# Performance work log

Measured on AMD Instinct MI355X. Metric: run time of the kernel, lower is better.

## Reference

```python
import jax, jax.numpy as jnp
import numpy as np

EPS = 1e-5
NUM_MEM_TOKENS = 16
SEGMENT_SIZE = 512


def dpfp(x):
    # DPFP feature map (Schlag et al.), nu=1: doubles the last dim, all-nonnegative.
    x2 = jnp.concatenate([jax.nn.relu(x), jax.nn.relu(-x)], axis=-1)
    return x2 * jnp.roll(x2, 1, axis=-1)


def setup_inputs() -> dict:
    key = jax.random.key(0)
    ks = jax.random.split(key, 7)
    B, S, D, DM = 4, 4224, 1024, 64  # S = n_seg * (segment_size + num_mem_tokens) = 8*528
    scale = 0.02
    return {
        "hidden_states": jax.random.normal(ks[0], (B, S, D), jnp.float32),
        "model_output": jax.random.normal(ks[1], (B, S, D), jnp.float32),
        "W_mq": jax.random.normal(ks[2], (D, DM), jnp.float32) * scale,
        "W_mk": jax.random.normal(ks[3], (D, DM), jnp.float32) * scale,
        "W_mv": jax.random.normal(ks[4], (D, D), jnp.float32) * scale,
        "W_mb": jax.random.normal(ks[5], (D, D), jnp.float32) * scale,
        "b_mb": jnp.zeros((D,), jnp.float32),
    }


def reference(hidden_states, model_output, W_mq, W_mk, W_mv, W_mb, b_mb):
    B, S, D = hidden_states.shape
    L = SEGMENT_SIZE + NUM_MEM_TOKENS
    n_seg = S // L
    d_key = 2 * W_mq.shape[1]  # dpfp doubles feature dim

    # [n_seg, B, L, D]
    h = hidden_states.reshape(B, n_seg, L, D).transpose(1, 0, 2, 3)
    m = model_output.reshape(B, n_seg, L, D).transpose(1, 0, 2, 3)

    def step(carry, seg):
        W_mem, z = carry  # [B, d_key, D], [B, d_key]
        hid, mo = seg     # [B, L, D] each
        # --- associate: linear-attention read of compressive memory ---
        q = dpfp(hid @ W_mq)                                   # [B, L, d_key]
        num = jnp.einsum('blk,bkd->bld', q, W_mem)             # [B, L, D]
        den = jnp.einsum('blk,bk->bl', q, z)[..., None] + EPS
        assoc = num / den
        # --- delta-rule memory update from memory tokens of segment output ---
        mem = (assoc + mo)[:, -NUM_MEM_TOKENS:]                # [B, M, D]
        k = dpfp(mem @ W_mk)                                   # [B, M, d_key]
        v = mem @ W_mv                                         # [B, M, D]
        gate = jax.nn.sigmoid(mem @ W_mb + b_mb)               # [B, M, D]
        prev = jnp.einsum('bmk,bkd->bmd', k, W_mem) / (
            jnp.einsum('bmk,bk->bm', k, z)[..., None] + EPS)   # correction (old value)
        new_info = gate * (v - prev)
        W_mem = W_mem + jnp.einsum('bmk,bmd->bkd', k, new_info)
        z = z + k.sum(axis=1)
        return (W_mem, z), assoc

    W0 = jnp.zeros((B, d_key, D), hidden_states.dtype)
    z0 = jnp.zeros((B, d_key), hidden_states.dtype)
    _, assocs = jax.lax.scan(step, (W0, z0), (h, m))           # [n_seg, B, L, D]
    association = jnp.tanh(assocs.transpose(1, 0, 2, 3).reshape(B, S, D))
    return model_output + association
```

## Files before the change

### kernel.cpp

```cpp
#include <hip/hip_runtime.h>
#include <hip/hip_bf16.h>

#define EPS 1e-5f

typedef short s8v __attribute__((ext_vector_type(8)));
typedef short s4v __attribute__((ext_vector_type(4)));
typedef float f4v __attribute__((ext_vector_type(4)));

__device__ __forceinline__ unsigned short f2bf(float f) {
  unsigned u = __builtin_bit_cast(unsigned, f);
  u = u + 0x7FFFu + ((u >> 16) & 1u);
  return (unsigned short)(u >> 16);
}
__device__ __forceinline__ float bf2f(unsigned short h) {
  unsigned u = ((unsigned)h) << 16;
  return __builtin_bit_cast(float, u);
}
__device__ __forceinline__ float fast_tanh(float x) {
  float e = __expf(2.0f * x);
  return 1.0f - 2.0f / (e + 1.0f);
}
__device__ __forceinline__ float fast_sigmoid(float x) {
  return 1.0f / (1.0f + __expf(-x));
}
__device__ __forceinline__ float frcp(float x) { return __builtin_amdgcn_rcpf(x); }

__global__ __launch_bounds__(256) void transpose_kernel(
    const float* __restrict__ W_mq, const float* __restrict__ W_mk,
    const float* __restrict__ W_mv, const float* __restrict__ W_mb,
    unsigned short* __restrict__ W_mqT, unsigned short* __restrict__ W_mkT,
    unsigned short* __restrict__ W_mvT, unsigned short* __restrict__ W_mbT) {
  __shared__ float tile[32][33];
  int bid = blockIdx.x;
  const float* src; unsigned short* dst; int N, t0;
  if (bid < 64)        { src = W_mq; dst = W_mqT; N = 64;   t0 = bid; }
  else if (bid < 128)  { src = W_mk; dst = W_mkT; N = 64;   t0 = bid - 64; }
  else if (bid < 1152) { src = W_mv; dst = W_mvT; N = 1024; t0 = bid - 128; }
  else                 { src = W_mb; dst = W_mbT; N = 1024; t0 = bid - 1152; }
  const int K = 1024;
  int tk = t0 & 31, tn = t0 >> 5;
  int k0 = tk * 32, n0 = tn * 32;
  int t = threadIdx.x;
  int cr = t >> 5, cc = t & 31;
#pragma unroll
  for (int u = 0; u < 4; u++) {
    int row = cr + u * 8;
    tile[row][cc] = src[(size_t)(k0 + row) * N + n0 + cc];
  }
  __syncthreads();
#pragma unroll
  for (int u = 0; u < 4; u++) {
    int nl = cr + u * 8;
    dst[(size_t)(n0 + nl) * K + k0 + cc] = f2bf(tile[cc][nl]);
  }
}

__global__ __launch_bounds__(128) void q_kernel(
    const float* __restrict__ HS, const unsigned short* __restrict__ W_mqT,
    unsigned short* __restrict__ Q) {
  __shared__ __align__(16) union { float y[16 * 64]; unsigned short kq[16 * 128]; } lds;
  int t = threadIdx.x, wv = t >> 6, lane = t & 63, m = lane & 15, q = lane >> 4;
  int r0 = blockIdx.x * 16;
  const float* ap = HS + (size_t)(r0 + m) * 1024 + wv * 512 + q * 8;
  const unsigned short* bp = W_mqT + (size_t)m * 1024 + wv * 512 + q * 8;
  f4v acc[4] = {f4v{0,0,0,0}, f4v{0,0,0,0}, f4v{0,0,0,0}, f4v{0,0,0,0}};
#pragma unroll 4
  for (int ks = 0; ks < 16; ks++) {
    int k0 = ks * 32;
    f4v h0 = *(const f4v*)(ap + k0);
    f4v h1 = *(const f4v*)(ap + k0 + 4);
    s8v a;
    a[0] = (short)f2bf(h0[0]); a[1] = (short)f2bf(h0[1]);
    a[2] = (short)f2bf(h0[2]); a[3] = (short)f2bf(h0[3]);
    a[4] = (short)f2bf(h1[0]); a[5] = (short)f2bf(h1[1]);
    a[6] = (short)f2bf(h1[2]); a[7] = (short)f2bf(h1[3]);
#pragma unroll
    for (int nf = 0; nf < 4; nf++) {
      s8v b = *(const s8v*)(bp + nf * 16384 + k0);
      acc[nf] = __builtin_amdgcn_mfma_f32_16x16x32_bf16(a, b, acc[nf], 0, 0, 0);
    }
  }
  if (wv == 1) {
#pragma unroll
    for (int nf = 0; nf < 4; nf++)
#pragma unroll
      for (int i = 0; i < 4; i++)
        lds.y[(nf * 4 + i) * 64 + lane] = acc[nf][i];
  }
  __syncthreads();
  if (wv == 0) {
#pragma unroll
    for (int nf = 0; nf < 4; nf++)
#pragma unroll
      for (int i = 0; i < 4; i++)
        acc[nf][i] += lds.y[(nf * 4 + i) * 64 + lane];
    int srcl = (lane & 48) | ((m + 15) & 15);
#pragma unroll
    for (int i = 0; i < 4; i++) {
      float yp[4];
#pragma unroll
      for (int nf = 0; nf < 4; nf++) yp[nf] = __shfl(acc[nf][i], srcl);
      int r = q * 4 + i;
#pragma unroll
      for (int nf = 0; nf < 4; nf++) {
        float yv = acc[nf][i];
        float py = (m != 0) ? yp[nf] : (nf > 0 ? yp[nf - 1] : yp[3]);
        bool wrap = (m == 0 && nf == 0);
        float x2lo = wrap ? fmaxf(-py, 0.f) : fmaxf(py, 0.f);
        float x2hi = wrap ? fmaxf(py, 0.f) : fmaxf(-py, 0.f);
        lds.kq[r * 128 + nf * 16 + m]      = f2bf(fmaxf(yv, 0.f) * x2lo);
        lds.kq[r * 128 + 64 + nf * 16 + m] = f2bf(fmaxf(-yv, 0.f) * x2hi);
      }
    }
  }
  __syncthreads();
  {
    int row = t >> 3, ch = t & 7;
    unsigned short* qp = Q + (size_t)(r0 + row) * 128 + ch * 16;
    *(s8v*)(qp)     = *(const s8v*)&lds.kq[row * 128 + ch * 16];
    *(s8v*)(qp + 8) = *(const s8v*)&lds.kq[row * 128 + ch * 16 + 8];
  }
}

__global__ __launch_bounds__(256, 1) void scan_kernel(
    const unsigned short* __restrict__ Qb, const unsigned short* __restrict__ W_mkT,
    const unsigned short* __restrict__ W_mvT, const unsigned short* __restrict__ W_mbT,
    const float* __restrict__ b_mb, const float* __restrict__ MO,
    float* __restrict__ OUT, unsigned short* __restrict__ hist,
    float* __restrict__ zh, unsigned short* __restrict__ mem_bf, int* bar) {
  __shared__ float Wf[128 * 64];
  __shared__ __align__(16) unsigned short Wbf[64 * 132];
  __shared__ float y_lds[16 * 64];
  __shared__ __align__(16) float k_f[16 * 128];
  __shared__ __align__(16) unsigned short k_bf[16 * 136];
  __shared__ float kden_l[16];
  __shared__ float ni_lds[16 * 65];
  __shared__ float z_l[128];

  int t = threadIdx.x, wv = t >> 6, lane = t & 63, m = lane & 15, q = lane >> 4;
  int ct = blockIdx.x & 15, b = blockIdx.x >> 4;
  int col = ct * 64 + wv * 16 + m;

  for (int i = t; i < 128 * 64; i += 256) Wf[i] = 0.f;
  for (int i = t; i < 64 * 132; i += 256) Wbf[i] = 0;
  if (t < 128) z_l[t] = 0.f;
  float bmb = b_mb[col];
  __syncthreads();

  s8v aq[4]; float mo_pf[4];
  {
    const unsigned short* qp = Qb + ((size_t)b * 4224 + 512 + m) * 128;
#pragma unroll
    for (int ks = 0; ks < 4; ks++) aq[ks] = *(const s8v*)(qp + ks * 32 + q * 8);
    const float* mop = MO + ((size_t)b * 4224 + 512 + q * 4) * 1024 + col;
#pragma unroll
    for (int i = 0; i < 4; i++) mo_pf[i] = mop[(size_t)i * 1024];
  }

  for (int s = 0; s < 8; s++) {
    {
      float dp = 0.f;
#pragma unroll
      for (int ks = 0; ks < 4; ks++)
#pragma unroll
        for (int j = 0; j < 8; j++)
          dp += bf2f((unsigned short)aq[ks][j]) * z_l[ks * 32 + q * 8 + j];
      dp += __shfl_xor(dp, 16);
      dp += __shfl_xor(dp, 32);
      dp += EPS;
      f4v acc = {0, 0, 0, 0};
#pragma unroll
      for (int ks = 0; ks < 4; ks++) {
        s8v bv = *(const s8v*)&Wbf[(wv * 16 + m) * 132 + ks * 32 + q * 8];
        acc = __builtin_amdgcn_mfma_f32_16x16x32_bf16(aq[ks], bv, acc, 0, 0, 0);
      }
      unsigned short* mb = mem_bf + (s & 1) * 65536 + b * 16384;
      size_t grow = (size_t)b * 4224 + s * 528 + 512;
#pragma unroll
      for (int i = 0; i < 4; i++) {
        float rden = frcp(__shfl(dp, q * 4 + i));
        float assoc = acc[i] * rden;
        float mov = mo_pf[i];
        OUT[(grow + q * 4 + i) * 1024 + col] = mov + fast_tanh(assoc);
        mb[(q * 4 + i) * 1024 + col] = f2bf(assoc + mov);
      }
    }
    __syncthreads();
    if (t == 0) {
      __threadfence();
      atomicAdd(bar + s * 4 + b, 1);
      while (__hip_atomic_load(bar + s * 4 + b, __ATOMIC_RELAXED,
                               __HIP_MEMORY_SCOPE_AGENT) < 16)
        __builtin_amdgcn_s_sleep(1);
      __threadfence();
    }
    __syncthreads();
    f4v accv = {0,0,0,0}, accg = {0,0,0,0};
    {
      const unsigned short* avp = mem_bf + (s & 1) * 65536 + b * 16384 + m * 1024 + q * 8;
      const unsigned short* bkp = W_mkT + (size_t)(wv * 16 + m) * 1024 + q * 8;
      const unsigned short* bvp = W_mvT + (size_t)col * 1024 + q * 8;
      const unsigned short* bgp = W_mbT + (size_t)col * 1024 + q * 8;
      f4v acy = {0, 0, 0, 0};
#pragma unroll 4
      for (int ks = 0; ks < 32; ks++) {
        s8v av = *(const s8v*)(avp + ks * 32);
        s8v bk = *(const s8v*)(bkp + ks * 32);
        s8v bv = *(const s8v*)(bvp + ks * 32);
        s8v bg = *(const s8v*)(bgp + ks * 32);
        acy  = __builtin_amdgcn_mfma_f32_16x16x32_bf16(av, bk, acy, 0, 0, 0);
        accv = __builtin_amdgcn_mfma_f32_16x16x32_bf16(av, bv, accv, 0, 0, 0);
        accg = __builtin_amdgcn_mfma_f32_16x16x32_bf16(av, bg, accg, 0, 0, 0);
      }
#pragma unroll
      for (int i = 0; i < 4; i++) y_lds[(q * 4 + i) * 64 + wv * 16 + m] = acy[i];
    }
    __syncthreads();
    {
      int r = t >> 4, jg = t & 15;
      const float* yr = &y_lds[r * 64];
      float pd = 0.f;
#pragma unroll
      for (int u = 0; u < 8; u++) {
        int jj = jg * 8 + u, jm = (jj + 127) & 127;
        float yj = (jj < 64) ? yr[jj] : -yr[jj - 64];
        float ym = (jm < 64) ? yr[jm] : -yr[jm - 64];
        float kv = fmaxf(yj, 0.f) * fmaxf(ym, 0.f);
        k_f[r * 128 + jj] = kv;
        k_bf[r * 136 + jj] = f2bf(kv);
        pd += kv * z_l[jj];
      }
      pd += __shfl_xor(pd, 1);
      pd += __shfl_xor(pd, 2);
      pd += __shfl_xor(pd, 4);
      pd += __shfl_xor(pd, 8);
      if (jg == 0) kden_l[r] = pd + EPS;
    }
    __syncthreads();
    {
      f4v accp = {0, 0, 0, 0};
#pragma unroll
      for (int ks = 0; ks < 4; ks++) {
        s8v ak = *(const s8v*)&k_bf[m * 136 + ks * 32 + q * 8];
        s8v bm = *(const s8v*)&Wbf[(wv * 16 + m) * 132 + ks * 32 + q * 8];
        accp = __builtin_amdgcn_mfma_f32_16x16x32_bf16(ak, bm, accp, 0, 0, 0);
      }
#pragma unroll
      for (int i = 0; i < 4; i++) {
        int r = q * 4 + i;
        float prev = accp[i] * frcp(kden_l[r]);
        float g = fast_sigmoid(accg[i] + bmb);
        ni_lds[r * 65 + wv * 16 + m] = g * (accv[i] - prev);
      }
      if (t < 128) {
        float ssum = 0.f;
#pragma unroll
        for (int r = 0; r < 16; r++) ssum += k_f[r * 128 + t];
        z_l[t] += ssum;
        if (s < 7) zh[(s + 1) * 512 + b * 128 + t] = z_l[t];
      }
    }
    __syncthreads();
    {
      int cl = t & 63, kg = t >> 6;
      float niv[16];
#pragma unroll
      for (int mm = 0; mm < 16; mm++) niv[mm] = ni_lds[mm * 65 + cl];
      float delta[32];
#pragma unroll
      for (int jj = 0; jj < 32; jj++) delta[jj] = 0.f;
#pragma unroll
      for (int mm = 0; mm < 16; mm++) {
        const float* kb = &k_f[mm * 128 + kg * 32];
        float nv = niv[mm];
#pragma unroll
        for (int ch = 0; ch < 8; ch++) {
          f4v kv4 = *(const f4v*)(kb + ch * 4);
#pragma unroll
          for (int jj = 0; jj < 4; jj++) delta[ch * 4 + jj] += kv4[jj] * nv;
        }
      }
      unsigned short* hdst = hist + (size_t)(s + 1) * 524288 +
                             ((size_t)b * 1024 + ct * 64 + cl) * 128 + kg * 32;
#pragma unroll
      for (int c8 = 0; c8 < 4; c8++) {
        s8v pk;
#pragma unroll
        for (int u = 0; u < 8; u++) {
          int kk = kg * 32 + c8 * 8 + u;
          float nv = Wf[kk * 64 + cl] + delta[c8 * 8 + u];
          Wf[kk * 64 + cl] = nv;
          pk[u] = (short)f2bf(nv);
        }
        *(s8v*)&Wbf[cl * 132 + kg * 32 + c8 * 8] = pk;
        if (s < 7) *(s8v*)(hdst + c8 * 8) = pk;
      }
      if (s < 7) {
        const unsigned short* qp = Qb + ((size_t)b * 4224 + (s + 1) * 528 + 512 + m) * 128;
#pragma unroll
        for (int ks = 0; ks < 4; ks++) aq[ks] = *(const s8v*)(qp + ks * 32 + q * 8);
        const float* mop = MO + ((size_t)b * 4224 + (s + 1) * 528 + 512 + q * 4) * 1024 + col;
#pragma unroll
        for (int i = 0; i < 4; i++) mo_pf[i] = mop[(size_t)i * 1024];
      }
    }
    __syncthreads();
  }
}

__global__ __launch_bounds__(256) void a_bulk_kernel(
    const unsigned short* __restrict__ Qb, const unsigned short* __restrict__ hist,
    const float* __restrict__ zh, const float* __restrict__ MO,
    float* __restrict__ OUT) {
  __shared__ float as_l[64 * 65];
  int t = threadIdx.x, wv = t >> 6, lane = t & 63, m = lane & 15, q = lane >> 4;
  int rt4 = blockIdx.x, ct = blockIdx.y;
  int seg = blockIdx.z >> 2, b = blockIdx.z & 3;
  const unsigned short* Wm = hist + (size_t)seg * 524288 + ((size_t)b * 1024 + ct * 64) * 128;
  const float* zp = zh + seg * 512 + b * 128;
  size_t grow = (size_t)b * 4224 + seg * 528 + rt4 * 64 + wv * 16;
  const unsigned short* qp = Qb + (grow + m) * 128;
  s8v a[4];
  float dp = 0.f;
#pragma unroll
  for (int ks = 0; ks < 4; ks++) {
    a[ks] = *(const s8v*)(qp + ks * 32 + q * 8);
    f4v z0 = *(const f4v*)(zp + ks * 32 + q * 8);
    f4v z1 = *(const f4v*)(zp + ks * 32 + q * 8 + 4);
#pragma unroll
    for (int j = 0; j < 4; j++) dp += bf2f((unsigned short)a[ks][j]) * z0[j];
#pragma unroll
    for (int j = 0; j < 4; j++) dp += bf2f((unsigned short)a[ks][j + 4]) * z1[j];
  }
  dp += __shfl_xor(dp, 16);
  dp += __shfl_xor(dp, 32);
  dp += EPS;
  f4v acc[4] = {f4v{0,0,0,0}, f4v{0,0,0,0}, f4v{0,0,0,0}, f4v{0,0,0,0}};
#pragma unroll
  for (int ks = 0; ks < 4; ks++) {
#pragma unroll
    for (int nf = 0; nf < 4; nf++) {
      s8v bv = *(const s8v*)(Wm + (size_t)(nf * 16 + m) * 128 + ks * 32 + q * 8);
      acc[nf] = __builtin_amdgcn_mfma_f32_16x16x32_bf16(a[ks], bv, acc[nf], 0, 0, 0);
    }
  }
#pragma unroll
  for (int i = 0; i < 4; i++) {
    float rden = frcp(__shfl(dp, q * 4 + i));
#pragma unroll
    for (int nf = 0; nf < 4; nf++)
      as_l[(wv * 16 + q * 4 + i) * 65 + nf * 16 + m] = acc[nf][i] * rden;
  }
  __syncthreads();
  {
    int r = t >> 2, cchunk = (t & 3) * 16;
    size_t rbase = ((size_t)b * 4224 + seg * 528 + rt4 * 64 + r) * 1024 + ct * 64 + cchunk;
    const float* ar = &as_l[r * 65 + cchunk];
#pragma unroll
    for (int u = 0; u < 4; u++) {
      f4v mo = *(const f4v*)(MO + rbase + u * 4);
      f4v o;
#pragma unroll
      for (int j = 0; j < 4; j++) o[j] = mo[j] + fast_tanh(ar[u * 4 + j]);
      *(f4v*)(OUT + rbase + u * 4) = o;
    }
  }
}

extern "C" void kernel_launch(void* const* d_in, const int* in_sizes, int n_in,
                              void* d_out, int out_size, void* d_ws, size_t ws_size,
                              hipStream_t stream) {
  const float* HS  = (const float*)d_in[0];
  const float* MO  = (const float*)d_in[1];
  const float* W_mq = (const float*)d_in[2];
  const float* W_mk = (const float*)d_in[3];
  const float* W_mv = (const float*)d_in[4];
  const float* W_mb = (const float*)d_in[5];
  const float* b_mb = (const float*)d_in[6];
  float* OUT = (float*)d_out;

  char* wsb = (char*)d_ws;
  unsigned short* hist   = (unsigned short*)(wsb + 0);
  float*          zh     = (float*)(wsb + 8388608);
  unsigned short* Qb     = (unsigned short*)(wsb + 8404992);
  unsigned short* W_mqT  = (unsigned short*)(wsb + 12730368);
  unsigned short* W_mkT  = (unsigned short*)(wsb + 12861440);
  unsigned short* W_mvT  = (unsigned short*)(wsb + 12992512);
  unsigned short* W_mbT  = (unsigned short*)(wsb + 15089664);
  unsigned short* mem_bf = (unsigned short*)(wsb + 17186816);
  int*            bar    = (int*)(wsb + 17448960);

  (void)hipMemsetAsync(wsb, 0, 1048576, stream);
  (void)hipMemsetAsync(wsb + 8388608, 0, 2048, stream);
  (void)hipMemsetAsync(bar, 0, 128, stream);
  transpose_kernel<<<2176, 256, 0, stream>>>(W_mq, W_mk, W_mv, W_mb,
                                             W_mqT, W_mkT, W_mvT, W_mbT);
  q_kernel<<<1056, 128, 0, stream>>>(HS, W_mqT, Qb);
  scan_kernel<<<64, 256, 0, stream>>>(Qb, W_mkT, W_mvT, W_mbT, b_mb, MO, OUT,
                                      hist, zh, mem_bf, bar);
  a_bulk_kernel<<<dim3(8, 16, 32), 256, 0, stream>>>(Qb, hist, zh, MO, OUT);
}
```

Baseline: 464.5 us.

## Fuse Q projection, scan, and bulk association into one persistent kernel with flags

```diff
diff --git a/kernel.cpp b/kernel.cpp
--- a/kernel.cpp
+++ b/kernel.cpp
@@ -4,7 +4,6 @@
 #define EPS 1e-5f
 
 typedef short s8v __attribute__((ext_vector_type(8)));
-typedef short s4v __attribute__((ext_vector_type(4)));
 typedef float f4v __attribute__((ext_vector_type(4)));
 
 __device__ __forceinline__ unsigned short f2bf(float f) {
@@ -55,12 +54,15 @@
   }
 }
 
-__global__ __launch_bounds__(128) void q_kernel(
-    const float* __restrict__ HS, const unsigned short* __restrict__ W_mqT,
-    unsigned short* __restrict__ Q) {
-  __shared__ __align__(16) union { float y[16 * 64]; unsigned short kq[16 * 128]; } lds;
-  int t = threadIdx.x, wv = t >> 6, lane = t & 63, m = lane & 15, q = lane >> 4;
-  int r0 = blockIdx.x * 16;
+union QLdsU { float y[16 * 64]; unsigned short kq[16 * 128]; };
+
+__device__ void q_tile_pair(const float* __restrict__ HS,
+                            const unsigned short* __restrict__ W_mqT,
+                            unsigned short* __restrict__ Q, int tile,
+                            char* qsmem) {
+  QLdsU* lds = (QLdsU*)qsmem;
+  int t = threadIdx.x & 127, wv = t >> 6, lane = t & 63, m = lane & 15, q = lane >> 4;
+  int r0 = tile * 16;
   const float* ap = HS + (size_t)(r0 + m) * 1024 + wv * 512 + q * 8;
   const unsigned short* bp = W_mqT + (size_t)m * 1024 + wv * 512 + q * 8;
   f4v acc[4] = {f4v{0,0,0,0}, f4v{0,0,0,0}, f4v{0,0,0,0}, f4v{0,0,0,0}};
@@ -85,7 +87,7 @@
     for (int nf = 0; nf < 4; nf++)
 #pragma unroll
       for (int i = 0; i < 4; i++)
-        lds.y[(nf * 4 + i) * 64 + lane] = acc[nf][i];
+        lds->y[(nf * 4 + i) * 64 + lane] = acc[nf][i];
   }
   __syncthreads();
   if (wv == 0) {
@@ -93,7 +95,7 @@
     for (int nf = 0; nf < 4; nf++)
 #pragma unroll
       for (int i = 0; i < 4; i++)
-        acc[nf][i] += lds.y[(nf * 4 + i) * 64 + lane];
+        acc[nf][i] += lds->y[(nf * 4 + i) * 64 + lane];
     int srcl = (lane & 48) | ((m + 15) & 15);
 #pragma unroll
     for (int i = 0; i < 4; i++) {
@@ -108,8 +110,8 @@
         bool wrap = (m == 0 && nf == 0);
         float x2lo = wrap ? fmaxf(-py, 0.f) : fmaxf(py, 0.f);
         float x2hi = wrap ? fmaxf(py, 0.f) : fmaxf(-py, 0.f);
-        lds.kq[r * 128 + nf * 16 + m]      = f2bf(fmaxf(yv, 0.f) * x2lo);
-        lds.kq[r * 128 + 64 + nf * 16 + m] = f2bf(fmaxf(-yv, 0.f) * x2hi);
+        lds->kq[r * 128 + nf * 16 + m]      = f2bf(fmaxf(yv, 0.f) * x2lo);
+        lds->kq[r * 128 + 64 + nf * 16 + m] = f2bf(fmaxf(-yv, 0.f) * x2hi);
       }
     }
   }
@@ -117,34 +119,50 @@
   {
     int row = t >> 3, ch = t & 7;
     unsigned short* qp = Q + (size_t)(r0 + row) * 128 + ch * 16;
-    *(s8v*)(qp)     = *(const s8v*)&lds.kq[row * 128 + ch * 16];
-    *(s8v*)(qp + 8) = *(const s8v*)&lds.kq[row * 128 + ch * 16 + 8];
-  }
-}
-
-__global__ __launch_bounds__(256, 1) void scan_kernel(
+    *(s8v*)(qp)     = *(const s8v*)&lds->kq[row * 128 + ch * 16];
+    *(s8v*)(qp + 8) = *(const s8v*)&lds->kq[row * 128 + ch * 16 + 8];
+  }
+}
+
+__device__ void scan_role(
+    const float* __restrict__ HS, const unsigned short* __restrict__ W_mqT,
     const unsigned short* __restrict__ Qb, const unsigned short* __restrict__ W_mkT,
     const unsigned short* __restrict__ W_mvT, const unsigned short* __restrict__ W_mbT,
     const float* __restrict__ b_mb, const float* __restrict__ MO,
     float* __restrict__ OUT, unsigned short* __restrict__ hist,
-    float* __restrict__ zh, unsigned short* __restrict__ mem_bf, int* bar) {
-  __shared__ float Wf[128 * 64];
-  __shared__ __align__(16) unsigned short Wbf[64 * 132];
-  __shared__ float y_lds[16 * 64];
-  __shared__ __align__(16) float k_f[16 * 128];
-  __shared__ __align__(16) unsigned short k_bf[16 * 136];
-  __shared__ float kden_l[16];
-  __shared__ float ni_lds[16 * 65];
-  __shared__ float z_l[128];
+    float* __restrict__ zh, unsigned short* __restrict__ mem_bf,
+    int* bar, int* qflags, char* smem) {
+  float* Wf           = (float*)smem;
+  unsigned short* Wbf = (unsigned short*)(smem + 32768);
+  float* y_lds        = (float*)(smem + 49664);
+  float* k_f          = (float*)(smem + 53760);
+  unsigned short* k_bf= (unsigned short*)(smem + 61952);
+  float* kden_l       = (float*)(smem + 66304);
+  float* ni_lds       = (float*)(smem + 66368);
+  float* z_l          = (float*)(smem + 70528);
 
   int t = threadIdx.x, wv = t >> 6, lane = t & 63, m = lane & 15, q = lane >> 4;
   int ct = blockIdx.x & 15, b = blockIdx.x >> 4;
   int col = ct * 64 + wv * 16 + m;
+
+  if (blockIdx.x < 16) {
+    int pair = t >> 7;
+    int sp = blockIdx.x * 2 + pair;
+    int tile = (sp >> 3) * 264 + (sp & 7) * 33 + 32;
+    q_tile_pair(HS, W_mqT, (unsigned short*)Qb, tile, smem + pair * 4096);
+    __syncthreads();
+    if (t == 0) { __threadfence(); atomicAdd(qflags, 2); }
+  }
 
   for (int i = t; i < 128 * 64; i += 256) Wf[i] = 0.f;
   for (int i = t; i < 64 * 132; i += 256) Wbf[i] = 0;
   if (t < 128) z_l[t] = 0.f;
   float bmb = b_mb[col];
+  if (t == 0) {
+    while (__hip_atomic_load(qflags, __ATOMIC_RELAXED, __HIP_MEMORY_SCOPE_AGENT) < 32)
+      __builtin_amdgcn_s_sleep(1);
+    __threadfence();
+  }
   __syncthreads();
 
   s8v aq[4]; float mo_pf[4];
@@ -308,62 +326,116 @@
   }
 }
 
-__global__ __launch_bounds__(256) void a_bulk_kernel(
-    const unsigned short* __restrict__ Qb, const unsigned short* __restrict__ hist,
+__device__ void worker_role(
+    const float* __restrict__ HS, const unsigned short* __restrict__ W_mqT,
+    unsigned short* __restrict__ Qb, const unsigned short* __restrict__ hist,
     const float* __restrict__ zh, const float* __restrict__ MO,
-    float* __restrict__ OUT) {
-  __shared__ float as_l[64 * 65];
-  int t = threadIdx.x, wv = t >> 6, lane = t & 63, m = lane & 15, q = lane >> 4;
-  int rt4 = blockIdx.x, ct = blockIdx.y;
-  int seg = blockIdx.z >> 2, b = blockIdx.z & 3;
-  const unsigned short* Wm = hist + (size_t)seg * 524288 + ((size_t)b * 1024 + ct * 64) * 128;
-  const float* zp = zh + seg * 512 + b * 128;
-  size_t grow = (size_t)b * 4224 + seg * 528 + rt4 * 64 + wv * 16;
-  const unsigned short* qp = Qb + (grow + m) * 128;
-  s8v a[4];
-  float dp = 0.f;
-#pragma unroll
-  for (int ks = 0; ks < 4; ks++) {
-    a[ks] = *(const s8v*)(qp + ks * 32 + q * 8);
-    f4v z0 = *(const f4v*)(zp + ks * 32 + q * 8);
-    f4v z1 = *(const f4v*)(zp + ks * 32 + q * 8 + 4);
-#pragma unroll
-    for (int j = 0; j < 4; j++) dp += bf2f((unsigned short)a[ks][j]) * z0[j];
-#pragma unroll
-    for (int j = 0; j < 4; j++) dp += bf2f((unsigned short)a[ks][j + 4]) * z1[j];
-  }
-  dp += __shfl_xor(dp, 16);
-  dp += __shfl_xor(dp, 32);
-  dp += EPS;
-  f4v acc[4] = {f4v{0,0,0,0}, f4v{0,0,0,0}, f4v{0,0,0,0}, f4v{0,0,0,0}};
-#pragma unroll
-  for (int ks = 0; ks < 4; ks++) {
-#pragma unroll
-    for (int nf = 0; nf < 4; nf++) {
-      s8v bv = *(const s8v*)(Wm + (size_t)(nf * 16 + m) * 128 + ks * 32 + q * 8);
-      acc[nf] = __builtin_amdgcn_mfma_f32_16x16x32_bf16(a[ks], bv, acc[nf], 0, 0, 0);
-    }
-  }
-#pragma unroll
-  for (int i = 0; i < 4; i++) {
-    float rden = frcp(__shfl(dp, q * 4 + i));
-#pragma unroll
-    for (int nf = 0; nf < 4; nf++)
-      as_l[(wv * 16 + q * 4 + i) * 65 + nf * 16 + m] = acc[nf][i] * rden;
+    float* __restrict__ OUT, int* bar, int* qflags, char* smem) {
+  int w = (int)blockIdx.x - 64;
+  int t = threadIdx.x;
+  int pair = t >> 7;
+  int np = 0;
+  for (int p = w; p < 512; p += 192) {
+    int rr = 2 * p + pair;
+    int tile = (rr >> 8) * 264 + ((rr & 255) >> 5) * 33 + (rr & 31);
+    q_tile_pair(HS, W_mqT, Qb, tile, smem + pair * 4096);
+    np++;
+    __syncthreads();
+  }
+  if (t == 0) { __threadfence(); atomicAdd(qflags + 1, np); }
+  for (int idx = w; idx < 512; idx += 192) {
+    int b = idx & 3, ct = (idx >> 2) & 15, rt4 = idx >> 6;
+    int r = t >> 2, cchunk = (t & 3) * 16;
+    size_t rbase = ((size_t)b * 4224 + (size_t)rt4 * 64 + r) * 1024 + ct * 64 + cchunk;
+#pragma unroll
+    for (int u = 0; u < 4; u++)
+      *(f4v*)(OUT + rbase + u * 4) = *(const f4v*)(MO + rbase + u * 4);
+  }
+  if (t == 0) {
+    while (__hip_atomic_load(qflags + 1, __ATOMIC_RELAXED, __HIP_MEMORY_SCOPE_AGENT) < 512)
+      __builtin_amdgcn_s_sleep(1);
+    __threadfence();
   }
   __syncthreads();
-  {
-    int r = t >> 2, cchunk = (t & 3) * 16;
-    size_t rbase = ((size_t)b * 4224 + seg * 528 + rt4 * 64 + r) * 1024 + ct * 64 + cchunk;
-    const float* ar = &as_l[r * 65 + cchunk];
-#pragma unroll
-    for (int u = 0; u < 4; u++) {
-      f4v mo = *(const f4v*)(MO + rbase + u * 4);
-      f4v o;
-#pragma unroll
-      for (int j = 0; j < 4; j++) o[j] = mo[j] + fast_tanh(ar[u * 4 + j]);
-      *(f4v*)(OUT + rbase + u * 4) = o;
-    }
+  int wv = t >> 6, lane = t & 63, m = lane & 15, q = lane >> 4;
+  float* as_l = (float*)smem;
+  for (int idx = 512 + w; idx < 4096; idx += 192) {
+    int seg = idx >> 9, inner = idx & 511;
+    int b = inner & 3, ct = (inner >> 2) & 15, rt4 = inner >> 6;
+    if (t == 0) {
+      while (__hip_atomic_load(bar + seg * 4 + b, __ATOMIC_RELAXED,
+                               __HIP_MEMORY_SCOPE_AGENT) < 16)
+        __builtin_amdgcn_s_sleep(2);
+      __threadfence();
+    }
+    __syncthreads();
+    const unsigned short* Wm = hist + (size_t)seg * 524288 + ((size_t)b * 1024 + ct * 64) * 128;
+    const float* zp = zh + seg * 512 + b * 128;
+    size_t grow = (size_t)b * 4224 + (size_t)seg * 528 + rt4 * 64 + wv * 16;
+    const unsigned short* qp = Qb + (grow + m) * 128;
+    s8v a[4];
+    float dp = 0.f;
+#pragma unroll
+    for (int ks = 0; ks < 4; ks++) {
+      a[ks] = *(const s8v*)(qp + ks * 32 + q * 8);
+      f4v z0 = *(const f4v*)(zp + ks * 32 + q * 8);
+      f4v z1 = *(const f4v*)(zp + ks * 32 + q * 8 + 4);
+#pragma unroll
+      for (int j = 0; j < 4; j++) dp += bf2f((unsigned short)a[ks][j]) * z0[j];
+#pragma unroll
+      for (int j = 0; j < 4; j++) dp += bf2f((unsigned short)a[ks][j + 4]) * z1[j];
+    }
+    dp += __shfl_xor(dp, 16);
+    dp += __shfl_xor(dp, 32);
+    dp += EPS;
+    f4v acc[4] = {f4v{0,0,0,0}, f4v{0,0,0,0}, f4v{0,0,0,0}, f4v{0,0,0,0}};
+#pragma unroll
+    for (int ks = 0; ks < 4; ks++) {
+#pragma unroll
+      for (int nf = 0; nf < 4; nf++) {
+        s8v bv = *(const s8v*)(Wm + (size_t)(nf * 16 + m) * 128 + ks * 32 + q * 8);
+        acc[nf] = __builtin_amdgcn_mfma_f32_16x16x32_bf16(a[ks], bv, acc[nf], 0, 0, 0);
+      }
+    }
+#pragma unroll
+    for (int i = 0; i < 4; i++) {
+      float rden = frcp(__shfl(dp, q * 4 + i));
+#pragma unroll
+      for (int nf = 0; nf < 4; nf++)
+        as_l[(wv * 16 + q * 4 + i) * 65 + nf * 16 + m] = acc[nf][i] * rden;
+    }
+    __syncthreads();
+    {
+      int r = t >> 2, cchunk = (t & 3) * 16;
+      size_t rbase = (grow - wv * 16 + r) * 1024 + ct * 64 + cchunk;
+      const float* ar = &as_l[r * 65 + cchunk];
+#pragma unroll
+      for (int u = 0; u < 4; u++) {
+        f4v mo = *(const f4v*)(MO + rbase + u * 4);
+        f4v o;
+#pragma unroll
+        for (int j = 0; j < 4; j++) o[j] = mo[j] + fast_tanh(ar[u * 4 + j]);
+        *(f4v*)(OUT + rbase + u * 4) = o;
+      }
+    }
+    __syncthreads();
+  }
+}
+
+__global__ __launch_bounds__(256, 1) void fused_kernel(
+    const float* __restrict__ HS, const unsigned short* __restrict__ W_mqT,
+    const unsigned short* __restrict__ W_mkT, const unsigned short* __restrict__ W_mvT,
+    const unsigned short* __restrict__ W_mbT, const float* __restrict__ b_mb,
+    const float* __restrict__ MO, float* __restrict__ OUT,
+    unsigned short* __restrict__ Qb, unsigned short* __restrict__ hist,
+    float* __restrict__ zh, unsigned short* __restrict__ mem_bf,
+    int* bar, int* qflags) {
+  __shared__ __align__(16) char smem[71040];
+  if (blockIdx.x < 64) {
+    scan_role(HS, W_mqT, Qb, W_mkT, W_mvT, W_mbT, b_mb, MO, OUT,
+              hist, zh, mem_bf, bar, qflags, smem);
+  } else {
+    worker_role(HS, W_mqT, Qb, hist, zh, MO, OUT, bar, qflags, smem);
   }
 }
 
@@ -389,14 +461,12 @@
   unsigned short* W_mbT  = (unsigned short*)(wsb + 15089664);
   unsigned short* mem_bf = (unsigned short*)(wsb + 17186816);
   int*            bar    = (int*)(wsb + 17448960);
-
-  (void)hipMemsetAsync(wsb, 0, 1048576, stream);
-  (void)hipMemsetAsync(wsb + 8388608, 0, 2048, stream);
+  int*            qflags = (int*)(wsb + 0);
+
+  (void)hipMemsetAsync(wsb, 0, 256, stream);
   (void)hipMemsetAsync(bar, 0, 128, stream);
   transpose_kernel<<<2176, 256, 0, stream>>>(W_mq, W_mk, W_mv, W_mb,
                                              W_mqT, W_mkT, W_mvT, W_mbT);
-  q_kernel<<<1056, 128, 0, stream>>>(HS, W_mqT, Qb);
-  scan_kernel<<<64, 256, 0, stream>>>(Qb, W_mkT, W_mvT, W_mbT, b_mb, MO, OUT,
-                                      hist, zh, mem_bf, bar);
-  a_bulk_kernel<<<dim3(8, 16, 32), 256, 0, stream>>>(Qb, hist, zh, MO, OUT);
-}
+  fused_kernel<<<256, 256, 0, stream>>>(HS, W_mqT, W_mkT, W_mvT, W_mbT, b_mb,
+                                        MO, OUT, Qb, hist, zh, mem_bf, bar, qflags);
+}
```

After: 527.9 us. +13.7%, slower.
